# Optimization experiments

Measured on AMD Instinct MI355X. Metric: run time of the kernel, lower is better.

## Reference

```python
import jax, jax.numpy as jnp
import numpy as np
from jax import lax

ITERS = 16
ALPHA = 0.3
SMOOTH = 1.0


def _maxpool3d(x, win):
    dims = (1, 1) + win
    return lax.reduce_window(x, -jnp.inf, lax.max, dims, (1,) * 5, 'SAME')


def soft_erode(x):
    # min-pool along each axis separately (clDice 3D soft erosion)
    e1 = -_maxpool3d(-x, (3, 1, 1))
    e2 = -_maxpool3d(-x, (1, 3, 1))
    e3 = -_maxpool3d(-x, (1, 1, 3))
    return jnp.minimum(jnp.minimum(e1, e2), e3)


def soft_dilate(x):
    return _maxpool3d(x, (3, 3, 3))


def soft_open(x):
    return soft_dilate(soft_erode(x))


def soft_skel(x, n_iter):
    skel = jax.nn.relu(x - soft_open(x))

    def body(carry, _):
        img, skel = carry
        img = soft_erode(img)
        delta = jax.nn.relu(img - soft_open(img))
        skel = skel + jax.nn.relu(delta - skel * delta)
        return (img, skel), None

    (_, skel), _ = lax.scan(body, (x, skel), None, length=n_iter)
    return skel


def soft_dice(y_true, y_pred, smooth):
    intersection = jnp.sum(y_true * y_pred)
    coeff = (2.0 * intersection + smooth) / (jnp.sum(y_true) + jnp.sum(y_pred) + smooth)
    return 1.0 - coeff


def setup_inputs() -> dict:
    key = jax.random.key(0)
    k1, k2 = jax.random.split(key)
    shape = (4, 1, 128, 128, 128)
    y_pred = jax.random.normal(k1, shape, dtype=jnp.float32)  # logits
    # binary ground-truth mask as float32
    y_true = jnp.round(jax.random.uniform(k2, shape, dtype=jnp.float32))
    return {"y_pred": y_pred, "y_true": y_true}


def reference(y_pred, y_true):
    yp = jax.nn.sigmoid(y_pred)
    dice = soft_dice(y_true, yp, SMOOTH)
    skel_pred = soft_skel(yp, ITERS)
    skel_true = soft_skel(y_true, ITERS)
    tprec = (jnp.sum(skel_pred * y_true) + SMOOTH) / (jnp.sum(skel_pred) + SMOOTH)
    tsens = (jnp.sum(skel_true * yp) + SMOOTH) / (jnp.sum(skel_true) + SMOOTH)
    cl_dice = 1.0 - 2.0 * (tprec * tsens) / (tprec + tsens)
    return (1.0 - ALPHA) * dice + ALPHA * cl_dice
```

## Files before the change

kernel.cpp:

```cpp
#include <hip/hip_runtime.h>
#include <cmath>

#define NB 4
#define ND 128
#define NH 128
#define NW 128
#define NVOL_VOX (ND * NH * NW)
#define NVOX (NB * NVOL_VOX)

#define THREADS 256
#define TX 32
#define TY 16
#define SSTR 18
#define RSTR 10
#define ZS4 ((NH * NW) >> 2)

__device__ __forceinline__ float4 f4min(float4 a, float4 b) {
    return make_float4(fminf(a.x, b.x), fminf(a.y, b.y), fminf(a.z, b.z), fminf(a.w, b.w));
}
__device__ __forceinline__ float4 f4max(float4 a, float4 b) {
    return make_float4(fmaxf(a.x, b.x), fmaxf(a.y, b.y), fmaxf(a.z, b.z), fmaxf(a.w, b.w));
}
__device__ __forceinline__ float4 f4relu_sub(float4 a, float4 b) {
    return make_float4(fmaxf(a.x - b.x, 0.f), fmaxf(a.y - b.y, 0.f),
                       fmaxf(a.z - b.z, 0.f), fmaxf(a.w - b.w, 0.f));
}
__device__ __forceinline__ float4 f4winmin_s(float lfw, float4 cc, float rtx) {
    float4 o;
    o.x = fminf(fminf(lfw, cc.x), cc.y);
    o.y = fminf(fminf(cc.x, cc.y), cc.z);
    o.z = fminf(fminf(cc.y, cc.z), cc.w);
    o.w = fminf(fminf(cc.z, cc.w), rtx);
    return o;
}
__device__ __forceinline__ float4 f4winmax_s(float lfw, float4 cc, float rtx) {
    float4 o;
    o.x = fmaxf(fmaxf(lfw, cc.x), cc.y);
    o.y = fmaxf(fmaxf(cc.x, cc.y), cc.z);
    o.z = fmaxf(fmaxf(cc.y, cc.z), cc.w);
    o.w = fmaxf(fmaxf(cc.z, cc.w), rtx);
    return o;
}

__device__ __forceinline__ float block_reduce(float v, float* sbuf) {
    for (int off = 32; off > 0; off >>= 1) v += __shfl_down(v, off, 64);
    int lane = threadIdx.x & 63;
    int wid  = threadIdx.x >> 6;
    if (lane == 0) sbuf[wid] = v;
    __syncthreads();
    float r = 0.f;
    if (wid == 0) {
        r = (lane < (int)(blockDim.x >> 6)) ? sbuf[lane] : 0.f;
        for (int off = 8; off > 0; off >>= 1) r += __shfl_down(r, off, 64);
    }
    __syncthreads();
    return r;
}

#define SIG_BLOCKS 1024
__global__ void sigmoid_reduce_kernel(const float4* __restrict__ logits,
                                      const float4* __restrict__ yt,
                                      float4* __restrict__ yp,
                                      float* __restrict__ part) {
    __shared__ float sbuf[THREADS / 64];
    const int n4 = NVOX / 4;
    float sp = 0.f, st = 0.f, stp = 0.f;
    for (int i = blockIdx.x * blockDim.x + threadIdx.x; i < n4;
         i += gridDim.x * blockDim.x) {
        float4 l = logits[i];
        float4 t = yt[i];
        float4 p;
        p.x = 1.f / (1.f + expf(-l.x));
        p.y = 1.f / (1.f + expf(-l.y));
        p.z = 1.f / (1.f + expf(-l.z));
        p.w = 1.f / (1.f + expf(-l.w));
        yp[i] = p;
        sp  += p.x + p.y + p.z + p.w;
        st  += t.x + t.y + t.z + t.w;
        stp += t.x * p.x + t.y * p.y + t.z * p.z + t.w * p.w;
    }
    float a = block_reduce(sp, sbuf);
    float b = block_reduce(st, sbuf);
    float c = block_reduce(stp, sbuf);
    if (threadIdx.x == 0) {
        part[blockIdx.x]        = a;
        part[1024 + blockIdx.x] = b;
        part[2048 + blockIdx.x] = c;
    }
}

template <int RED, int INIT>
__global__ __launch_bounds__(256, 2)
void skel_pair_kernel(const float* __restrict__ srcA, const float* __restrict__ srcB,
                      float* __restrict__ imgOut, float* __restrict__ skel,
                      int zchunks,
                      const float* __restrict__ othA, const float* __restrict__ othB,
                      float* __restrict__ part, int offBase) {
    __shared__ float4 srcS[2][24 * SSTR];
    __shared__ float4 e1S [2][22 * SSTR];
    __shared__ float4 e2S [2][20 * SSTR];
    __shared__ float4 e3S [2][18 * SSTR];
    __shared__ float4 rxAS[2][18 * RSTR];
    __shared__ float4 rxBS[2][18 * RSTR];
    __shared__ float4 rxCS[2][INIT ? 18 * RSTR : 1];

    const float4 INF4  = make_float4(INFINITY, INFINITY, INFINITY, INFINITY);
    const float4 MINF4 = make_float4(-INFINITY, -INFINITY, -INFINITY, -INFINITY);
    const float4 ZERO4 = make_float4(0.f, 0.f, 0.f, 0.f);

    const int zlen  = ND / zchunks;
    const int v     = blockIdx.z / zchunks;
    const int chunk = blockIdx.z - v * zchunks;
    const int z0    = chunk * zlen;
    const int tx0   = blockIdx.x * TX;
    const int ty0   = blockIdx.y * TY;
    const int tid   = threadIdx.x;

    const float* src = srcB ? (v < 4 ? srcA + (size_t)v * NVOL_VOX
                                     : srcB + (size_t)(v - 4) * NVOL_VOX)
                            : srcA + (size_t)v * NVOL_VOX;
    const float4* src4 = (const float4*)src;
    float4* img4 = imgOut ? (float4*)(imgOut + (size_t)v * NVOL_VOX) : nullptr;
    float4* skl4 = (float4*)(skel + (size_t)v * NVOL_VOX);
    const float4* oth4 = nullptr;
    if (RED) {
        const float* oth = othB ? (v < 4 ? othA + (size_t)v * NVOL_VOX
                                         : othB + (size_t)(v - 4) * NVOL_VOX)
                                : othA + (size_t)v * NVOL_VOX;
        oth4 = (const float4*)oth;
    }

    const int fy = tid / 10, qx = tid - (tid / 10) * 10;
    const bool tOK = tid < 240;
    const bool aE1 = tOK && fy >= 1 && fy < 23;
    const bool aE2 = tOK && fy >= 2 && fy < 22;
    const bool aE3 = tOK && fy >= 3 && fy < 21;
    const bool aRx = aE3 && qx >= 1 && qx < 9;
    const bool aC  = tOK && fy >= 4 && fy < 20 && qx >= 1 && qx < 9;
    const int gy = ty0 + fy - 4;
    const int gx4 = tx0 + (qx - 1) * 4;
    const bool gOK = tOK && (unsigned)gy < NH && (unsigned)gx4 < NW;
    const int colBase = gOK ? ((gy * NW + gx4) >> 2) : 0;
    const int iSrc = fy * SSTR + qx + 1;
    const int iE1  = (fy - 1) * SSTR + qx + 1;
    const int iE2  = (fy - 2) * SSTR + qx + 1;
    const int iE3  = (fy - 3) * SSTR + qx + 1;
    const int iRx  = (fy - 3) * RSTR + (qx - 1);

    for (int l = tid; l < 2 * 24 * 2; l += THREADS)
        srcS[l & 1][(l >> 2) * SSTR + ((l >> 1) & 1) * 11] = INF4;
    for (int l = tid; l < 2 * 22 * 2; l += THREADS)
        e1S[l & 1][(l >> 2) * SSTR + ((l >> 1) & 1) * 11] = INF4;
    for (int l = tid; l < 2 * 20 * 2; l += THREADS)
        e2S[l & 1][(l >> 2) * SSTR + ((l >> 1) & 1) * 11] = INF4;
    for (int l = tid; l < 2 * 18 * 2; l += THREADS)
        e3S[l & 1][(l >> 2) * SSTR + ((l >> 1) & 1) * 11] = INF4;
    __syncthreads();

    constexpr int SD = INIT ? 6 : 3;
    float4 srcF[SD], e1F[6], e2F[6], e3F[2], rxAF[2], rxBF[2], mxyAF[3], mxyBF[3], dAF[2];
    float4 sklF[6], othF[6];
    float4 rxCF[2], mxyCF[3], d0F[3];
#pragma unroll
    for (int i = 0; i < SD; ++i) srcF[i] = INF4;
#pragma unroll
    for (int i = 0; i < 6; ++i) { e1F[i] = INF4; e2F[i] = INF4; sklF[i] = ZERO4; othF[i] = ZERO4; }
    e3F[0] = e3F[1] = INF4;
    rxAF[0] = rxAF[1] = MINF4;
    rxBF[0] = rxBF[1] = MINF4;
    rxCF[0] = rxCF[1] = MINF4;
    mxyAF[0] = mxyAF[1] = mxyAF[2] = MINF4;
    mxyBF[0] = mxyBF[1] = mxyBF[2] = MINF4;
    mxyCF[0] = mxyCF[1] = mxyCF[2] = MINF4;
    dAF[0] = dAF[1] = ZERO4;
    d0F[0] = d0F[1] = d0F[2] = ZERO4;

    float accS = 0.f, accSO = 0.f;
    const int NSTEP = zlen + 10;

    for (int sb = 0; sb < NSTEP; sb += 6) {
#pragma unroll
        for (int u = 0; u < 6; ++u) {
            if (sb + u >= NSTEP) break;
            const int zL = z0 - 4 + (sb + u);
            const int sl  = u & 1;
            const int slp = sl ^ 1;

            {
                float4 vv = INF4;
                if ((unsigned)zL < ND && zL < z0 + zlen + 4 && gOK)
                    vv = src4[zL * ZS4 + colBase];
                srcF[u % SD] = vv;
                if (tOK) srcS[sl][iSrc] = vv;
            }
            if (!INIT) {
                const int zp = zL - 3;
                const bool pOK = aC && zp >= z0 && zp < z0 + zlen;
                float4 sv = ZERO4;
                if (pOK) sv = skl4[zp * ZS4 + colBase];
                sklF[u] = sv;
                if (RED) {
                    float4 ov = ZERO4;
                    if (pOK) ov = oth4[zp * ZS4 + colBase];
                    othF[u] = ov;
                }
            }
            {
                const int z = zL - 1;
                float4 vv = INF4;
                if (aE1 && (unsigned)z < ND) {
                    const float4* S = srcS[slp];
                    const float* fS = (const float*)S;
                    float4 cc = INIT ? srcF[(u + 5) % 6] : srcF[(u + 2) % SD];
                    float4 zm = INIT ? f4min(srcF[(u + 4) % 6], srcF[u % 6])
                                     : f4min(srcF[(u + 1) % SD], srcF[u % SD]);
                    float4 xm = f4winmin_s(fS[4 * iSrc - 1], cc, fS[4 * iSrc + 4]);
                    vv = f4min(f4min(xm, S[iSrc - SSTR]),
                               f4min(S[iSrc + SSTR], zm));
                }
                e1F[u % 6] = vv;
                if (aE1) e1S[sl][iE1] = vv;
            }
            {
                const int z = zL - 2;
                float4 vv = INF4;
                if (aE2) {
                    const float4* S = e1S[slp];
                    const float* fS = (const float*)S;
                    float4 xm = f4winmin_s(fS[4 * iE1 - 1], e1F[(u + 5) % 6], fS[4 * iE1 + 4]);
                    vv = f4min(f4min(xm, S[iE1 - SSTR]),
                               f4min(S[iE1 + SSTR],
                                     f4min(e1F[(u + 4) % 6], e1F[u % 6])));
                    e2S[sl][iE2] = vv;
                    if (img4 && aC && z >= z0 && z < z0 + zlen)
                        img4[z * ZS4 + colBase] = vv;
                }
                e2F[u % 6] = vv;
            }
            {
                float4 vv = INF4;
                if (aE3) {
                    const float4* S = e2S[slp];
                    const float* fS = (const float*)S;
                    float4 xm = f4winmin_s(fS[4 * iE2 - 1], e2F[(u + 5) % 6], fS[4 * iE2 + 4]);
                    vv = f4min(f4min(xm, S[iE2 - SSTR]),
                               f4min(S[iE2 + SSTR],
                                     f4min(e2F[(u + 4) % 6], e2F[u % 6])));
                    e3S[sl][iE3] = vv;
                }
                e3F[u % 2] = vv;
            }
            {
                float4 ra = MINF4, rb = MINF4, rc = MINF4;
                if (aRx) {
                    const float* fA = (const float*)e2S[slp];
                    const float* fB = (const float*)e3S[slp];
                    ra = f4winmax_s(fA[4 * iE2 - 1], e2F[(u + 5) % 6], fA[4 * iE2 + 4]);
                    rb = f4winmax_s(fB[4 * iE3 - 1], e3F[(u + 1) % 2], fB[4 * iE3 + 4]);
                    rxAS[sl][iRx] = ra;
                    rxBS[sl][iRx] = rb;
                    if (INIT) {
                        const float* fC = (const float*)e1S[slp];
                        rc = f4winmax_s(fC[4 * iE1 - 1], e1F[(u + 5) % 6], fC[4 * iE1 + 4]);
                        rxCS[sl][iRx] = rc;
                    }
                }
                float4 mA = MINF4, mB = MINF4, mC = MINF4;
                if (aC) {
                    mA = f4max(f4max(rxAF[(u + 1) % 2], rxAS[slp][iRx - RSTR]),
                               rxAS[slp][iRx + RSTR]);
                    mB = f4max(f4max(rxBF[(u + 1) % 2], rxBS[slp][iRx - RSTR]),
                               rxBS[slp][iRx + RSTR]);
                    if (INIT)
                        mC = f4max(f4max(rxCF[(u + 1) % 2], rxCS[slp][iRx - RSTR]),
                                   rxCS[slp][iRx + RSTR]);
                }
                rxAF[u % 2] = ra;
                rxBF[u % 2] = rb;
                mxyAF[u % 3] = mA;
                mxyBF[u % 3] = mB;
                if (INIT) { rxCF[u % 2] = rc; mxyCF[u % 3] = mC; }
            }
            if (INIT) {
                float4 dilC = f4max(f4max(mxyCF[0], mxyCF[1]), mxyCF[2]);
                d0F[u % 3] = f4relu_sub(srcF[(u + 2) % 6], dilC);
            }
            {
                float4 dilA = f4max(f4max(mxyAF[0], mxyAF[1]), mxyAF[2]);
                dAF[u % 2] = f4relu_sub(e1F[(u + 2) % 6], dilA);
            }
            {
                const int z = zL - 6;
                if (aC && z >= z0 && z < z0 + zlen) {
                    float4 dilB = f4max(f4max(mxyBF[0], mxyBF[1]), mxyBF[2]);
                    float4 dB = f4relu_sub(e2F[(u + 2) % 6], dilB);
                    float4 da = dAF[(u + 1) % 2];
                    int gi = z * ZS4 + colBase;
                    float4 sv = INIT ? d0F[(u + 1) % 3] : sklF[(u + 3) % 6];
                    float4 s1, s2;
                    s1.x = sv.x + fmaxf(da.x - sv.x * da.x, 0.f);
                    s1.y = sv.y + fmaxf(da.y - sv.y * da.y, 0.f);
                    s1.z = sv.z + fmaxf(da.z - sv.z * da.z, 0.f);
                    s1.w = sv.w + fmaxf(da.w - sv.w * da.w, 0.f);
                    s2.x = s1.x + fmaxf(dB.x - s1.x * dB.x, 0.f);
                    s2.y = s1.y + fmaxf(dB.y - s1.y * dB.y, 0.f);
                    s2.z = s1.z + fmaxf(dB.z - s1.z * dB.z, 0.f);
                    s2.w = s1.w + fmaxf(dB.w - s1.w * dB.w, 0.f);
                    skl4[gi] = s2;
                    if (RED) {
                        accS += s2.x + s2.y + s2.z + s2.w;
                        float4 o = othF[(u + 3) % 6];
                        accSO += s2.x * o.x + s2.y * o.y + s2.z * o.z + s2.w * o.w;
                    }
                }
            }
            __syncthreads();
        }
    }

    if (RED) {
        float* sbuf = (float*)srcS;
        float r1 = block_reduce(accS, sbuf);
        float r2 = block_reduce(accSO, sbuf);
        if (tid == 0) {
            int halfSel = (othB && v >= 4) ? 1 : 0;
            int A = (offBase + 2 * halfSel) * 1024;
            int zslot = chunk + zchunks * (v & 3);
            int bid = blockIdx.x + 4 * (blockIdx.y + 8 * zslot);
            part[A + bid] = r1;
            part[A + 1024 + bid] = r2;
        }
    }
}

__global__ void finalize_kernel(const float* __restrict__ part, float* __restrict__ out) {
    __shared__ float sbuf[THREADS / 64];
    float s[7];
#pragma unroll
    for (int k = 0; k < 7; ++k) {
        float local = 0.f;
        for (int i = threadIdx.x; i < 1024; i += THREADS) local += part[k * 1024 + i];
        s[k] = block_reduce(local, sbuf);
    }
    if (threadIdx.x == 0) {
        const float smooth = 1.0f;
        const float alpha = 0.3f;
        float dice = 1.f - (2.f * s[2] + smooth) / (s[1] + s[0] + smooth);
        float tprec = (s[4] + smooth) / (s[3] + smooth);
        float tsens = (s[6] + smooth) / (s[5] + smooth);
        float cl = 1.f - 2.f * (tprec * tsens) / (tprec + tsens);
        out[0] = (1.f - alpha) * dice + alpha * cl;
    }
}

extern "C" void kernel_launch(void* const* d_in, const int* in_sizes, int n_in,
                              void* d_out, int out_size, void* d_ws, size_t ws_size,
                              hipStream_t stream) {
    const float* y_pred = (const float*)d_in[0];
    const float* y_true = (const float*)d_in[1];
    float* out = (float*)d_out;

    char* ws = (char*)d_ws;
    float* part = (float*)ws;
    float* yp = (float*)(ws + 32768);
    const size_t NB4 = (size_t)NVOX;
    const size_t need_batched = 32768 + 7 * NB4 * sizeof(float);

    hipMemsetAsync(part, 0, 7 * 1024 * sizeof(float), stream);
    sigmoid_reduce_kernel<<<SIG_BLOCKS, THREADS, 0, stream>>>(
        (const float4*)y_pred, (const float4*)y_true, (float4*)yp, part);

    if (ws_size >= need_batched) {
        float* ping = yp + NB4;
        float* pong = ping + 2 * NB4;
        float* S    = pong + 2 * NB4;
        const int zc = 2;
        dim3 grid(NW / TX, NH / TY, zc * 8);

        skel_pair_kernel<0, 1><<<grid, THREADS, 0, stream>>>(
            yp, y_true, ping, S, zc, nullptr, nullptr, nullptr, 0);

        float* bufs[2] = {ping, pong};
        for (int j = 0; j < 7; ++j) {
            const float* sA = bufs[j & 1];
            float* oimg = (j < 6) ? bufs[(j + 1) & 1] : nullptr;
            if (j < 6)
                skel_pair_kernel<0, 0><<<grid, THREADS, 0, stream>>>(
                    sA, nullptr, oimg, S, zc, nullptr, nullptr, nullptr, 0);
            else
                skel_pair_kernel<1, 0><<<grid, THREADS, 0, stream>>>(
                    sA, nullptr, oimg, S, zc, y_true, yp, part, 3);
        }
    } else {
        float* ping = yp + NB4;
        float* pong = ping + NB4;
        float* Sp   = pong + NB4;
        float* St   = Sp + NB4;
        const int zc = 4;
        dim3 grid(NW / TX, NH / TY, zc * 4);

        auto run = [&](const float* x, float* S, const float* other, int offBase) {
            skel_pair_kernel<0, 1><<<grid, THREADS, 0, stream>>>(
                x, nullptr, ping, S, zc, nullptr, nullptr, nullptr, 0);
            float* bufs[2] = {ping, pong};
            for (int j = 0; j < 7; ++j) {
                const float* sA = bufs[j & 1];
                float* oimg = (j < 6) ? bufs[(j + 1) & 1] : nullptr;
                if (j < 6)
                    skel_pair_kernel<0, 0><<<grid, THREADS, 0, stream>>>(
                        sA, nullptr, oimg, S, zc, nullptr, nullptr, nullptr, 0);
                else
                    skel_pair_kernel<1, 0><<<grid, THREADS, 0, stream>>>(
                        sA, nullptr, oimg, S, zc, other, nullptr, part, offBase);
            }
        };
        run(yp, Sp, y_true, 3);
        run(y_true, St, yp, 5);
    }

    finalize_kernel<<<1, THREADS, 0, stream>>>(part, out);
}
```

Before: 946.5 us.

## Shrink shared-memory tiles, raise occupancy target, and split z into more chunks

Cuts the shared-memory row stride from 18 to 10 float4 by dropping the padded infinity halo columns, and replaces them with per-thread edge selects on the left and right neighbour reads. The buffers are packed into one flat array, launch bounds ask for 4 blocks per SM instead of 2, and z is split into 4 chunks to double the grid. The aim is higher occupancy and more parallelism. In exchange there is more redundant halo recomputation per z chunk and more register pressure under the tighter launch bound.

Measured after the change: 1.665 ms. +75.9%, slower.

```diff
diff --git a/kernel.cpp b/kernel.cpp
--- a/kernel.cpp
+++ b/kernel.cpp
@@ -11,9 +11,11 @@
 #define THREADS 256
 #define TX 32
 #define TY 16
-#define SSTR 18
+#define SSTR 10
 #define RSTR 10
 #define ZS4 ((NH * NW) >> 2)
+
+#define INFF __builtin_huge_valf()
 
 __device__ __forceinline__ float4 f4min(float4 a, float4 b) {
     return make_float4(fminf(a.x, b.x), fminf(a.y, b.y), fminf(a.z, b.z), fminf(a.w, b.w));
@@ -90,22 +92,30 @@
 }
 
 template <int RED, int INIT>
-__global__ __launch_bounds__(256, 2)
+__global__ __launch_bounds__(256, 4)
 void skel_pair_kernel(const float* __restrict__ srcA, const float* __restrict__ srcB,
                       float* __restrict__ imgOut, float* __restrict__ skel,
                       int zchunks,
                       const float* __restrict__ othA, const float* __restrict__ othB,
                       float* __restrict__ part, int offBase) {
-    __shared__ float4 srcS[2][24 * SSTR];
-    __shared__ float4 e1S [2][22 * SSTR];
-    __shared__ float4 e2S [2][20 * SSTR];
-    __shared__ float4 e3S [2][18 * SSTR];
-    __shared__ float4 rxAS[2][18 * RSTR];
-    __shared__ float4 rxBS[2][18 * RSTR];
-    __shared__ float4 rxCS[2][INIT ? 18 * RSTR : 1];
-
-    const float4 INF4  = make_float4(INFINITY, INFINITY, INFINITY, INFINITY);
-    const float4 MINF4 = make_float4(-INFINITY, -INFINITY, -INFINITY, -INFINITY);
+    constexpr int ZSRC = 24 * SSTR;
+    constexpr int ZE1  = 22 * SSTR;
+    constexpr int ZE2  = 20 * SSTR;
+    constexpr int ZE3  = 18 * SSTR;
+    constexpr int ZRX  = 18 * RSTR;
+    constexpr int NTOT = 2 + 2 * (ZSRC + ZE1 + ZE2 + ZE3 + 2 * ZRX)
+                           + (INIT ? 2 * ZRX : 0);
+    __shared__ float4 smem[NTOT];
+    float4* const srcS = smem + 1;
+    float4* const e1S  = srcS + 2 * ZSRC;
+    float4* const e2S  = e1S + 2 * ZE1;
+    float4* const e3S  = e2S + 2 * ZE2;
+    float4* const rxAS = e3S + 2 * ZE3;
+    float4* const rxBS = rxAS + 2 * ZRX;
+    float4* const rxCS = rxBS + 2 * ZRX;
+
+    const float4 INF4  = make_float4(INFF, INFF, INFF, INFF);
+    const float4 MINF4 = make_float4(-INFF, -INFF, -INFF, -INFF);
     const float4 ZERO4 = make_float4(0.f, 0.f, 0.f, 0.f);
 
     const int zlen  = ND / zchunks;
@@ -137,25 +147,17 @@
     const bool aE3 = tOK && fy >= 3 && fy < 21;
     const bool aRx = aE3 && qx >= 1 && qx < 9;
     const bool aC  = tOK && fy >= 4 && fy < 20 && qx >= 1 && qx < 9;
+    const bool qxL = (qx == 0);
+    const bool qxR = (qx == 9);
     const int gy = ty0 + fy - 4;
     const int gx4 = tx0 + (qx - 1) * 4;
     const bool gOK = tOK && (unsigned)gy < NH && (unsigned)gx4 < NW;
     const int colBase = gOK ? ((gy * NW + gx4) >> 2) : 0;
-    const int iSrc = fy * SSTR + qx + 1;
-    const int iE1  = (fy - 1) * SSTR + qx + 1;
-    const int iE2  = (fy - 2) * SSTR + qx + 1;
-    const int iE3  = (fy - 3) * SSTR + qx + 1;
+    const int iSrc = fy * SSTR + qx;
+    const int iE1  = (fy - 1) * SSTR + qx;
+    const int iE2  = (fy - 2) * SSTR + qx;
+    const int iE3  = (fy - 3) * SSTR + qx;
     const int iRx  = (fy - 3) * RSTR + (qx - 1);
-
-    for (int l = tid; l < 2 * 24 * 2; l += THREADS)
-        srcS[l & 1][(l >> 2) * SSTR + ((l >> 1) & 1) * 11] = INF4;
-    for (int l = tid; l < 2 * 22 * 2; l += THREADS)
-        e1S[l & 1][(l >> 2) * SSTR + ((l >> 1) & 1) * 11] = INF4;
-    for (int l = tid; l < 2 * 20 * 2; l += THREADS)
-        e2S[l & 1][(l >> 2) * SSTR + ((l >> 1) & 1) * 11] = INF4;
-    for (int l = tid; l < 2 * 18 * 2; l += THREADS)
-        e3S[l & 1][(l >> 2) * SSTR + ((l >> 1) & 1) * 11] = INF4;
-    __syncthreads();
 
     constexpr int SD = INIT ? 6 : 3;
     float4 srcF[SD], e1F[6], e2F[6], e3F[2], rxAF[2], rxBF[2], mxyAF[3], mxyBF[3], dAF[2];
@@ -191,7 +193,7 @@
                 if ((unsigned)zL < ND && zL < z0 + zlen + 4 && gOK)
                     vv = src4[zL * ZS4 + colBase];
                 srcF[u % SD] = vv;
-                if (tOK) srcS[sl][iSrc] = vv;
+                if (tOK) srcS[sl * ZSRC + iSrc] = vv;
             }
             if (!INIT) {
                 const int zp = zL - 3;
@@ -209,29 +211,33 @@
                 const int z = zL - 1;
                 float4 vv = INF4;
                 if (aE1 && (unsigned)z < ND) {
-                    const float4* S = srcS[slp];
+                    const float4* S = srcS + slp * ZSRC;
                     const float* fS = (const float*)S;
                     float4 cc = INIT ? srcF[(u + 5) % 6] : srcF[(u + 2) % SD];
                     float4 zm = INIT ? f4min(srcF[(u + 4) % 6], srcF[u % 6])
                                      : f4min(srcF[(u + 1) % SD], srcF[u % SD]);
-                    float4 xm = f4winmin_s(fS[4 * iSrc - 1], cc, fS[4 * iSrc + 4]);
+                    float lfw = qxL ? INFF : fS[4 * iSrc - 1];
+                    float rtx = qxR ? INFF : fS[4 * iSrc + 4];
+                    float4 xm = f4winmin_s(lfw, cc, rtx);
                     vv = f4min(f4min(xm, S[iSrc - SSTR]),
                                f4min(S[iSrc + SSTR], zm));
                 }
                 e1F[u % 6] = vv;
-                if (aE1) e1S[sl][iE1] = vv;
+                if (aE1) e1S[sl * ZE1 + iE1] = vv;
             }
             {
                 const int z = zL - 2;
                 float4 vv = INF4;
                 if (aE2) {
-                    const float4* S = e1S[slp];
+                    const float4* S = e1S + slp * ZE1;
                     const float* fS = (const float*)S;
-                    float4 xm = f4winmin_s(fS[4 * iE1 - 1], e1F[(u + 5) % 6], fS[4 * iE1 + 4]);
+                    float lfw = qxL ? INFF : fS[4 * iE1 - 1];
+                    float rtx = qxR ? INFF : fS[4 * iE1 + 4];
+                    float4 xm = f4winmin_s(lfw, e1F[(u + 5) % 6], rtx);
                     vv = f4min(f4min(xm, S[iE1 - SSTR]),
                                f4min(S[iE1 + SSTR],
                                      f4min(e1F[(u + 4) % 6], e1F[u % 6])));
-                    e2S[sl][iE2] = vv;
+                    e2S[sl * ZE2 + iE2] = vv;
                     if (img4 && aC && z >= z0 && z < z0 + zlen)
                         img4[z * ZS4 + colBase] = vv;
                 }
@@ -240,40 +246,42 @@
             {
                 float4 vv = INF4;
                 if (aE3) {
-                    const float4* S = e2S[slp];
+                    const float4* S = e2S + slp * ZE2;
                     const float* fS = (const float*)S;
-                    float4 xm = f4winmin_s(fS[4 * iE2 - 1], e2F[(u + 5) % 6], fS[4 * iE2 + 4]);
+                    float lfw = qxL ? INFF : fS[4 * iE2 - 1];
+                    float rtx = qxR ? INFF : fS[4 * iE2 + 4];
+                    float4 xm = f4winmin_s(lfw, e2F[(u + 5) % 6], rtx);
                     vv = f4min(f4min(xm, S[iE2 - SSTR]),
                                f4min(S[iE2 + SSTR],
                                      f4min(e2F[(u + 4) % 6], e2F[u % 6])));
-                    e3S[sl][iE3] = vv;
+                    e3S[sl * ZE3 + iE3] = vv;
                 }
                 e3F[u % 2] = vv;
             }
             {
                 float4 ra = MINF4, rb = MINF4, rc = MINF4;
                 if (aRx) {
-                    const float* fA = (const float*)e2S[slp];
-                    const float* fB = (const float*)e3S[slp];
+                    const float* fA = (const float*)(e2S + slp * ZE2);
+                    const float* fB = (const float*)(e3S + slp * ZE3);
                     ra = f4winmax_s(fA[4 * iE2 - 1], e2F[(u + 5) % 6], fA[4 * iE2 + 4]);
                     rb = f4winmax_s(fB[4 * iE3 - 1], e3F[(u + 1) % 2], fB[4 * iE3 + 4]);
-                    rxAS[sl][iRx] = ra;
-                    rxBS[sl][iRx] = rb;
+                    rxAS[sl * ZRX + iRx] = ra;
+                    rxBS[sl * ZRX + iRx] = rb;
                     if (INIT) {
-                        const float* fC = (const float*)e1S[slp];
+                        const float* fC = (const float*)(e1S + slp * ZE1);
                         rc = f4winmax_s(fC[4 * iE1 - 1], e1F[(u + 5) % 6], fC[4 * iE1 + 4]);
-                        rxCS[sl][iRx] = rc;
+                        rxCS[sl * ZRX + iRx] = rc;
                     }
                 }
                 float4 mA = MINF4, mB = MINF4, mC = MINF4;
                 if (aC) {
-                    mA = f4max(f4max(rxAF[(u + 1) % 2], rxAS[slp][iRx - RSTR]),
-                               rxAS[slp][iRx + RSTR]);
-                    mB = f4max(f4max(rxBF[(u + 1) % 2], rxBS[slp][iRx - RSTR]),
-                               rxBS[slp][iRx + RSTR]);
+                    mA = f4max(f4max(rxAF[(u + 1) % 2], rxAS[slp * ZRX + iRx - RSTR]),
+                               rxAS[slp * ZRX + iRx + RSTR]);
+                    mB = f4max(f4max(rxBF[(u + 1) % 2], rxBS[slp * ZRX + iRx - RSTR]),
+                               rxBS[slp * ZRX + iRx + RSTR]);
                     if (INIT)
-                        mC = f4max(f4max(rxCF[(u + 1) % 2], rxCS[slp][iRx - RSTR]),
-                                   rxCS[slp][iRx + RSTR]);
+                        mC = f4max(f4max(rxCF[(u + 1) % 2], rxCS[slp * ZRX + iRx - RSTR]),
+                                   rxCS[slp * ZRX + iRx + RSTR]);
                 }
                 rxAF[u % 2] = ra;
                 rxBF[u % 2] = rb;
@@ -319,7 +327,7 @@
     }
 
     if (RED) {
-        float* sbuf = (float*)srcS;
+        float* sbuf = (float*)smem;
         float r1 = block_reduce(accS, sbuf);
         float r2 = block_reduce(accSO, sbuf);
         if (tid == 0) {
@@ -374,7 +382,7 @@
         float* ping = yp + NB4;
         float* pong = ping + 2 * NB4;
         float* S    = pong + 2 * NB4;
-        const int zc = 2;
+        const int zc = 4;
         dim3 grid(NW / TX, NH / TY, zc * 8);
 
         skel_pair_kernel<0, 1><<<grid, THREADS, 0, stream>>>(
```
